# Kernel tuning notes

Hardware: AMD Instinct MI355X
Metric: run time of the kernel (lower is better)

## Reference

```python
import jax, jax.numpy as jnp
import numpy as np

L = 3          # layers
D = 256        # hidden_dim
H = 4          # heads
F = 1024       # ffn_size
IMG = (64, 32) # img_dim
S = IMG[0] * IMG[1]
DK = D // H    # key/query head dim
V = 2 * D      # double_v_dim value dim
DV = V // H    # value head dim
B = 2


def _rel_pos():
    # rotary angles, repeated pairwise as in get_rel_pos
    angle = 1.0 / (10000.0 ** jnp.linspace(0.0, 1.0, DK // 2))
    angle = jnp.repeat(angle, 2)                                  # [DK]
    idx = jnp.arange(S, dtype=jnp.float32)
    sin = jnp.sin(idx[:, None] * angle[None, :])                  # [S, DK]
    cos = jnp.cos(idx[:, None] * angle[None, :])
    # per-head causal decay mask, row-normalized by sqrt(rowsum)
    decay = jnp.log(1.0 - 2.0 ** (-5.0 - jnp.arange(H, dtype=jnp.float32)))  # [H]
    diff = idx[:, None] - idx[None, :]                            # [S, S]
    mask = jnp.where(diff >= 0, jnp.exp(diff[None, :, :] * decay[:, None, None]), 0.0)
    mask = mask / jnp.sqrt(mask.sum(-1, keepdims=True))           # [H, S, S]
    return sin, cos, mask


def _theta_shift(x, sin, cos):
    # x: [B, H, S, DK]; rotate-every-two rotary embedding
    x1, x2 = x[..., ::2], x[..., 1::2]
    rot = jnp.stack([-x2, x1], axis=-1).reshape(x.shape)
    return x * cos + rot * sin


def _ln(x, w, b, eps=1e-5):
    mu = x.mean(-1, keepdims=True)
    var = ((x - mu) ** 2).mean(-1, keepdims=True)
    return (x - mu) / jnp.sqrt(var + eps) * w + b


def _retention(x, sin, cos, mask, Wq, Wk, Wv, Wg, Wo):
    b, s, _ = x.shape
    q = (x @ Wq).reshape(b, s, H, DK).transpose(0, 2, 1, 3)
    k = (x @ Wk).reshape(b, s, H, DK).transpose(0, 2, 1, 3) * (DK ** -0.5)
    v = (x @ Wv).reshape(b, s, H, DV).transpose(0, 2, 1, 3)
    g = x @ Wg                                                    # [b, s, V]
    qr = _theta_shift(q, sin, cos)
    kr = _theta_shift(k, sin, cos)
    qk = jnp.einsum('bhsd,bhtd->bhst', qr, kr) * mask[None]
    denom = jnp.clip(jnp.abs(qk).sum(-1, keepdims=True), 1.0, None)
    qk = qk / jax.lax.stop_gradient(denom)
    o = jnp.einsum('bhst,bhtv->bhsv', qk, v)                      # [b, H, s, DV]
    o = o * jax.lax.rsqrt((o ** 2).mean(-1, keepdims=True) + 1e-6)  # per-head RMSNorm
    o = o.transpose(0, 2, 1, 3).reshape(b, s, V)
    o = (g * jax.nn.sigmoid(g)) * o                               # swish gate
    return o @ Wo


def setup_inputs():
    key = jax.random.key(0)
    ks = jax.random.split(key, 16)
    sc = 0.02
    return {
        'x': jax.random.normal(ks[0], (B, S, D), jnp.float32),
        'Wq': jax.random.normal(ks[1], (L, D, D), jnp.float32) * sc,
        'Wk': jax.random.normal(ks[2], (L, D, D), jnp.float32) * sc,
        'Wv': jax.random.normal(ks[3], (L, D, V), jnp.float32) * sc,
        'Wg': jax.random.normal(ks[4], (L, D, V), jnp.float32) * sc,
        'Wo': jax.random.normal(ks[5], (L, V, D), jnp.float32) * sc,
        'ln1_w': jnp.ones((L, D), jnp.float32),
        'ln1_b': jnp.zeros((L, D), jnp.float32),
        'ln2_w': jnp.ones((L, D), jnp.float32),
        'ln2_b': jnp.zeros((L, D), jnp.float32),
        'W1': jax.random.normal(ks[6], (L, D, F), jnp.float32) * sc,
        'b1': jnp.zeros((L, F), jnp.float32),
        'W2': jax.random.normal(ks[7], (L, F, D), jnp.float32) * sc,
        'b2': jnp.zeros((L, D), jnp.float32),
    }


def reference(x, Wq, Wk, Wv, Wg, Wo, ln1_w, ln1_b, ln2_w, ln2_b, W1, b1, W2, b2):
    sin, cos, mask = _rel_pos()
    for i in range(L):
        y = _retention(_ln(x, ln1_w[i], ln1_b[i]), sin, cos, mask,
                       Wq[i], Wk[i], Wv[i], Wg[i], Wo[i]) + x
        h = _ln(y, ln2_w[i], ln2_b[i])
        x = (jax.nn.gelu(h @ W1[i] + b1[i], approximate=False) @ W2[i] + b2[i]) + y
    return x.reshape(x.shape[0], IMG[0], IMG[1], D)
```

## Files before the change

kernel.cpp:

```cpp
#include <hip/hip_runtime.h>
#include <hip/hip_bf16.h>
#include <cstddef>
#include <cmath>
#include <algorithm>

#define SEQ 2048
#define DMODEL 256
#define NHEAD 4
#define DK 64
#define VDIM 512
#define DV 128
#define NB 2
#define FDIM 1024
#define NROWS (NB*SEQ)
#define QKVGN 1536
#define NSLOT 144

typedef unsigned short u16;
typedef __attribute__((ext_vector_type(8))) short short8;
typedef __attribute__((ext_vector_type(4))) short short4v;
typedef __attribute__((ext_vector_type(4))) float f32x4;

static __device__ __forceinline__ u16 f2b(float f) {
    union { float f; unsigned u; } c; c.f = f;
    unsigned r = c.u + 0x7fffu + ((c.u >> 16) & 1u);
    return (u16)(r >> 16);
}
static __device__ __forceinline__ float b2f(u16 u) {
    union { unsigned u; float f; } c; c.u = ((unsigned)u) << 16; return c.f;
}

static __device__ __forceinline__ f32x4 mfma16_bf16(short4v a, short4v b, f32x4 c) {
    return __builtin_amdgcn_mfma_f32_16x16x16bf16_1k(a, b, c, 0, 0, 0);
}

static __device__ __forceinline__ short4v pack_bf16x4(float a0, float a1, float a2, float a3) {
    union { short4v v; unsigned u[2]; } z;
    union { __hip_bfloat162 h; unsigned u; } p0, p1;
    p0.h = __float22bfloat162_rn(make_float2(a0, a1));
    p1.h = __float22bfloat162_rn(make_float2(a2, a3));
    z.u[0] = p0.u; z.u[1] = p1.u;
    return z.v;
}

#define GLOAD_LDS16(GP, LP) \
    __builtin_amdgcn_global_load_lds((const __attribute__((address_space(1))) void*)(GP), \
                                     (__attribute__((address_space(3))) void*)(LP), 16, 0, 0)

__global__ void tables_kernel(float* __restrict__ sint, float* __restrict__ cost)
{
    int idx = blockIdx.x * 256 + threadIdx.x;
    if (idx >= SEQ * DK) return;
    int s = idx >> 6, d = idx & 63;
    int j = d >> 1;
    float a = powf(10000.f, -(float)j / 31.f);
    float arg = (float)s * a;
    sint[idx] = sinf(arg);
    cost[idx] = cosf(arg);
}

__global__ __launch_bounds__(256) void wconv_kernel(const float* __restrict__ in,
                                                    u16* __restrict__ out, int K, int N,
                                                    size_t in_lstride, size_t out_lstride)
{
    __shared__ float tile[32][33];
    int n0 = blockIdx.x * 32, k0 = blockIdx.y * 32;
    const float* inz = in + (size_t)blockIdx.z * in_lstride;
    u16* outz = out + (size_t)blockIdx.z * out_lstride;
    int tx = threadIdx.x, ty = threadIdx.y;
    #pragma unroll
    for (int r = 0; r < 4; ++r) {
        int kr = ty + r * 8;
        tile[kr][tx] = inz[(size_t)(k0 + kr) * N + n0 + tx];
    }
    __syncthreads();
    #pragma unroll
    for (int r = 0; r < 4; ++r) {
        int nr = ty + r * 8;
        outz[(size_t)(n0 + nr) * K + k0 + tx] = f2b(tile[tx][nr]);
    }
}

__global__ __launch_bounds__(256) void ln_kernel(const float* __restrict__ x,
                                                 const float* __restrict__ w,
                                                 const float* __restrict__ b,
                                                 u16* __restrict__ o)
{
    int row = blockIdx.x;
    int t = threadIdx.x;
    float v = x[(size_t)row * DMODEL + t];
    __shared__ float red[256];
    red[t] = v; __syncthreads();
    for (int st = 128; st > 0; st >>= 1) { if (t < st) red[t] += red[t + st]; __syncthreads(); }
    float mu = red[0] * (1.f / DMODEL);
    __syncthreads();
    red[t] = v * v; __syncthreads();
    for (int st = 128; st > 0; st >>= 1) { if (t < st) red[t] += red[t + st]; __syncthreads(); }
    float var = red[0] * (1.f / DMODEL) - mu * mu;
    o[(size_t)row * DMODEL + t] = f2b((v - mu) * rsqrtf(var + 1e-5f) * w[t] + b[t]);
}

template<int NPART, int HASBIAS>
__global__ __launch_bounds__(256) void lncomb_kernel(const u16* __restrict__ pW,
                                                     const float* __restrict__ bias,
                                                     const float* __restrict__ res,
                                                     const float* __restrict__ w,
                                                     const float* __restrict__ b,
                                                     float* __restrict__ yout,
                                                     u16* __restrict__ o)
{
    int row = blockIdx.x;
    int t = threadIdx.x;
    size_t i = (size_t)row * DMODEL + t;
    const size_t PS = (size_t)NROWS * DMODEL;
    float v = res[i];
    #pragma unroll
    for (int k = 0; k < NPART; ++k) v += b2f(pW[i + k * PS]);
    if (HASBIAS) v += bias[t];
    yout[i] = v;
    __shared__ float red[256];
    red[t] = v; __syncthreads();
    for (int st = 128; st > 0; st >>= 1) { if (t < st) red[t] += red[t + st]; __syncthreads(); }
    float mu = red[0] * (1.f / DMODEL);
    __syncthreads();
    red[t] = v * v; __syncthreads();
    for (int st = 128; st > 0; st >>= 1) { if (t < st) red[t] += red[t + st]; __syncthreads(); }
    float var = red[0] * (1.f / DMODEL) - mu * mu;
    o[i] = f2b((v - mu) * rsqrtf(var + 1e-5f) * w[t] + b[t]);
}

__global__ __launch_bounds__(256) void comb4_kernel(const u16* __restrict__ pW,
                                                    const float* __restrict__ bias,
                                                    const float* __restrict__ yb,
                                                    float* __restrict__ out)
{
    int row = blockIdx.x;
    int t = threadIdx.x;
    size_t i = (size_t)row * DMODEL + t;
    const size_t PS = (size_t)NROWS * DMODEL;
    out[i] = b2f(pW[i]) + b2f(pW[i + PS]) + b2f(pW[i + 2 * PS]) + b2f(pW[i + 3 * PS]) + bias[t] + yb[i];
}

template<int BIAS, int GELU, int ROT, int OUTBF, int SPLIT, int VT>
__global__ __launch_bounds__(256) void gemm64(const u16* __restrict__ A,
                                              const u16* __restrict__ Bt,
                                              void* __restrict__ Cout,
                                              const float* __restrict__ bias,
                                              const float* __restrict__ sint,
                                              const float* __restrict__ cost,
                                              u16* __restrict__ vtout,
                                              int M, int N, int K, int kslice)
{
    __shared__ __align__(16) u16 As[64 * 64];
    __shared__ __align__(16) u16 Bs[64 * 64];
    int bx = blockIdx.x, by = blockIdx.y;
    int tid = threadIdx.x;
    int wave = tid >> 6, lane = tid & 63;
    int wm = wave & 1, wn = wave >> 1;
    int l15 = lane & 15, lg = lane >> 4;
    int kb0 = SPLIT ? blockIdx.z * kslice : 0;
    int kcnt = SPLIT ? kslice : K;

    int L0 = wave * 64 + lane;
    int r0 = L0 >> 3, c0g = (L0 & 7) ^ ((r0 >> 1) & 7);
    int L1 = 256 + wave * 64 + lane;
    int r1 = L1 >> 3, c1g = (L1 & 7) ^ ((r1 >> 1) & 7);
    const u16* Ag0 = A + (size_t)(by * 64 + r0) * K + kb0 + c0g * 8;
    const u16* Ag1 = A + (size_t)(by * 64 + r1) * K + kb0 + c1g * 8;
    const u16* Bg0 = Bt + (size_t)(bx * 64 + r0) * K + kb0 + c0g * 8;
    const u16* Bg1 = Bt + (size_t)(bx * 64 + r1) * K + kb0 + c1g * 8;
    u16* Asw0 = &As[wave * 512];
    u16* Asw1 = &As[2048 + wave * 512];
    u16* Bsw0 = &Bs[wave * 512];
    u16* Bsw1 = &Bs[2048 + wave * 512];

    f32x4 acc[2][2] = {};
    for (int k0 = 0; k0 < kcnt; k0 += 64) {
        GLOAD_LDS16(Ag0 + k0, Asw0);
        GLOAD_LDS16(Ag1 + k0, Asw1);
        GLOAD_LDS16(Bg0 + k0, Bsw0);
        GLOAD_LDS16(Bg1 + k0, Bsw1);
        __syncthreads();
        #pragma unroll
        for (int kk = 0; kk < 2; ++kk) {
            short8 af[2], bf[2];
            #pragma unroll
            for (int i = 0; i < 2; ++i) {
                int ra = wm * 32 + i * 16 + l15;
                int rb = wn * 32 + i * 16 + l15;
                af[i] = *(const short8*)&As[ra * 64 + ((kk * 4 + lg) ^ ((ra >> 1) & 7)) * 8];
                bf[i] = *(const short8*)&Bs[rb * 64 + ((kk * 4 + lg) ^ ((rb >> 1) & 7)) * 8];
            }
            #pragma unroll
            for (int mi = 0; mi < 2; ++mi)
                #pragma unroll
                for (int ni = 0; ni < 2; ++ni)
                    acc[mi][ni] = __builtin_amdgcn_mfma_f32_16x16x32_bf16(af[mi], bf[ni], acc[mi][ni], 0, 0, 0);
        }
        __syncthreads();
    }

    float* Cf = (float*)Cout;
    u16* Ch = (u16*)Cout;
    u16* Chs = (u16*)Cout;
    #pragma unroll
    for (int mi = 0; mi < 2; ++mi)
        #pragma unroll
        for (int ni = 0; ni < 2; ++ni) {
            int colb = bx * 64 + wn * 32 + ni * 16;
            if (VT && colb >= 512 && colb < 1024) {
                int col = colb + l15;
                int z = ((by >> 5) << 2) + ((col - 512) >> 7);
                int dv = (col - 512) & 127;
                int s0b = (by * 64 + wm * 32) & (SEQ - 1);
                short4v pk = pack_bf16x4(acc[mi][ni][0], acc[mi][ni][1], acc[mi][ni][2], acc[mi][ni][3]);
                *(short4v*)(vtout + (size_t)(z * DV + dv) * SEQ + s0b + lg * 8 + mi * 4) = pk;
            } else {
                #pragma unroll
                for (int r = 0; r < 4; ++r) {
                    int row = by * 64 + wm * 32 + mi * 16 + lg * 4 + r;
                    int col = colb + l15;
                    float v = acc[mi][ni][r];
                    if (ROT) {
                        float pv = __shfl_xor(v, 1);
                        if (col < 512) {
                            int s = row & (SEQ - 1);
                            int dk = col & 63;
                            float c = cost[(s << 6) + dk], sn = sint[(s << 6) + dk];
                            float rv = (col & 1) ? (v * c + pv * sn) : (v * c - pv * sn);
                            v = (col < 256) ? rv : rv * 0.125f;
                        }
                    }
                    if (BIAS) v += bias[col];
                    if (GELU) v = 0.5f * v * (1.f + erff(v * 0.70710678118654752f));
                    if (SPLIT)      Chs[(size_t)blockIdx.z * M * N + (size_t)row * N + col] = f2b(v);
                    else if (OUTBF) Ch[(size_t)row * N + col] = f2b(v);
                    else            Cf[(size_t)row * N + col] = v;
                }
            }
        }
}

__global__ __launch_bounds__(256) void retention_p1(
    const u16* __restrict__ qkvg, const u16* __restrict__ vt,
    u16* __restrict__ po, float* __restrict__ pden)
{
    __shared__ __align__(16) u16 Klds[2][2048];
    __shared__ __align__(16) u16 Vlds[2][4096];

    int bid = blockIdx.x;
    int bh = bid & 7;
    int f = bid >> 3;
    int a = 0, base = 0;
    while (f >= base + 4 * (a + 1)) { base += 4 * (a + 1); ++a; }
    int segs = f - base;
    int qt64 = 4 * a + segs / (a + 1);
    int ch = segs % (a + 1);
    int b = bh >> 2, h = bh & 3;
    int slot = bh * NSLOT + f;

    int tid = threadIdx.x;
    int wave = tid >> 6, lane = tid & 63;
    int wq = wave;
    int l15 = lane & 15, lg = lane >> 4;

    float rgeo = 1.f - exp2f(-5.f - (float)h);
    float dec2 = log2f(rgeo);
    float step = exp2f(dec2 * -32.f);

    const u16* qbase  = qkvg + (size_t)b * SEQ * QKVGN + h * 64;
    const u16* kbase  = qbase + 256;
    const u16* vtg    = vt + (size_t)bh * DV * SEQ;

    int q0w = qt64 * 64 + wq * 16;
    short8 qf0 = *(const short8*)(qbase + (size_t)(q0w + l15) * QKVGN + lg * 8);
    short8 qf1 = *(const short8*)(qbase + (size_t)(q0w + l15) * QKVGN + 32 + lg * 8);

    int tb = ch * 8;
    int t_last = (ch == a) ? (2 * qt64 + 1) : (tb + 7);
    int hasdiag = (ch == a);

    float rinv  = exp2f(-dec2);
    float r16   = exp2f(dec2 * -16.f);
    float et00 = exp2f(dec2 * -(float)(tb * 32 + lg * 4));
    float et01 = et00 * rinv;
    float et02 = et01 * rinv;
    float et03 = et02 * rinv;
    float et10 = et00 * r16, et11 = et01 * r16, et12 = et02 * r16, et13 = et03 * r16;

    f32x4 oacc0 = {0.f,0.f,0.f,0.f}, oacc1 = {0.f,0.f,0.f,0.f};
    f32x4 oacc2 = {0.f,0.f,0.f,0.f}, oacc3 = {0.f,0.f,0.f,0.f};
    f32x4 oacc4 = {0.f,0.f,0.f,0.f}, oacc5 = {0.f,0.f,0.f,0.f};
    f32x4 oacc6 = {0.f,0.f,0.f,0.f}, oacc7 = {0.f,0.f,0.f,0.f};
    float den_l = 0.f;

#define STAGE(BUF, TI) do { \
    int t0_ = (TI) * 32; \
    _Pragma("unroll") \
    for (int ii = 0; ii < 3; ++ii) { \
        int inst_ = wave * 3 + ii; \
        if (inst_ < 4) { \
            const u16* g_ = kbase + (size_t)(t0_ + (lane & 31)) * QKVGN + (2 * inst_ + (lane >> 5)) * 8; \
            GLOAD_LDS16(g_, &Klds[BUF][inst_ * 512]); \
        } else { \
            int j_ = inst_ - 4; \
            const u16* g_ = vtg + (size_t)(j_ * 16 + (lane >> 2)) * SEQ + t0_ + (lane & 3) * 8; \
            GLOAD_LDS16(g_, &Vlds[BUF][j_ * 512]); \
        } \
    } \
} while (0)

#define PVSTEP(PA, SEL0, SEL1, SEL2, SEL3, SEL4, SEL5, SEL6, SEL7) do { \
    oacc0 = mfma16_bf16(PA, __builtin_shufflevector(V0, V0, SEL0, SEL1, SEL2, SEL3), oacc0); \
    oacc1 = mfma16_bf16(PA, __builtin_shufflevector(V1, V1, SEL0, SEL1, SEL2, SEL3), oacc1); \
    oacc2 = mfma16_bf16(PA, __builtin_shufflevector(V2, V2, SEL0, SEL1, SEL2, SEL3), oacc2); \
    oacc3 = mfma16_bf16(PA, __builtin_shufflevector(V3, V3, SEL0, SEL1, SEL2, SEL3), oacc3); \
    oacc4 = mfma16_bf16(PA, __builtin_shufflevector(V4, V4, SEL0, SEL1, SEL2, SEL3), oacc4); \
    oacc5 = mfma16_bf16(PA, __builtin_shufflevector(V5, V5, SEL0, SEL1, SEL2, SEL3), oacc5); \
    oacc6 = mfma16_bf16(PA, __builtin_shufflevector(V6, V6, SEL0, SEL1, SEL2, SEL3), oacc6); \
    oacc7 = mfma16_bf16(PA, __builtin_shufflevector(V7, V7, SEL0, SEL1, SEL2, SEL3), oacc7); \
} while (0)

#define BODY(BUF, T0, DIAG) do { \
    const u16* kb_ = &Klds[BUF][0]; \
    const u16* vb_ = &Vlds[BUF][0]; \
    short8 k00 = *(const short8*)(kb_ + (lg    ) * 256 + l15 * 8); \
    short8 k01 = *(const short8*)(kb_ + (4 + lg) * 256 + l15 * 8); \
    short8 k10 = *(const short8*)(kb_ + (lg    ) * 256 + (16 + l15) * 8); \
    short8 k11 = *(const short8*)(kb_ + (4 + lg) * 256 + (16 + l15) * 8); \
    short8 V0 = *(const short8*)(vb_ + (      l15) * 32 + lg * 8); \
    short8 V1 = *(const short8*)(vb_ + (16 +  l15) * 32 + lg * 8); \
    short8 V2 = *(const short8*)(vb_ + (32 +  l15) * 32 + lg * 8); \
    short8 V3 = *(const short8*)(vb_ + (48 +  l15) * 32 + lg * 8); \
    short8 V4 = *(const short8*)(vb_ + (64 +  l15) * 32 + lg * 8); \
    short8 V5 = *(const short8*)(vb_ + (80 +  l15) * 32 + lg * 8); \
    short8 V6 = *(const short8*)(vb_ + (96 +  l15) * 32 + lg * 8); \
    short8 V7 = *(const short8*)(vb_ + (112 + l15) * 32 + lg * 8); \
    f32x4 s0 = {0.f,0.f,0.f,0.f}, s1 = {0.f,0.f,0.f,0.f}; \
    s0 = __builtin_amdgcn_mfma_f32_16x16x32_bf16(k00, qf0, s0, 0, 0, 0); \
    s0 = __builtin_amdgcn_mfma_f32_16x16x32_bf16(k01, qf1, s0, 0, 0, 0); \
    s1 = __builtin_amdgcn_mfma_f32_16x16x32_bf16(k10, qf0, s1, 0, 0, 0); \
    s1 = __builtin_amdgcn_mfma_f32_16x16x32_bf16(k11, qf1, s1, 0, 0, 0); \
    float a0 = s0[0] * et00, a1 = s0[1] * et01, a2 = s0[2] * et02, a3 = s0[3] * et03; \
    float c0 = s1[0] * et10, c1 = s1[1] * et11, c2 = s1[2] * et12, c3 = s1[3] * et13; \
    if (DIAG) { \
        int qr_ = q0w + l15; \
        int tg_ = (T0) + lg * 4; \
        a0 = (tg_ +  0 <= qr_) ? a0 : 0.f;  a1 = (tg_ +  1 <= qr_) ? a1 : 0.f; \
        a2 = (tg_ +  2 <= qr_) ? a2 : 0.f;  a3 = (tg_ +  3 <= qr_) ? a3 : 0.f; \
        c0 = (tg_ + 16 <= qr_) ? c0 : 0.f;  c1 = (tg_ + 17 <= qr_) ? c1 : 0.f; \
        c2 = (tg_ + 18 <= qr_) ? c2 : 0.f;  c3 = (tg_ + 19 <= qr_) ? c3 : 0.f; \
    } \
    den_l += fabsf(a0) + fabsf(a1) + fabsf(a2) + fabsf(a3) \
           + fabsf(c0) + fabsf(c1) + fabsf(c2) + fabsf(c3); \
    short4v pa0 = pack_bf16x4(a0, a1, a2, a3); \
    short4v pa1 = pack_bf16x4(c0, c1, c2, c3); \
    PVSTEP(pa0, 0, 1, 2, 3, 0, 0, 0, 0); \
    PVSTEP(pa1, 4, 5, 6, 7, 0, 0, 0, 0); \
    et00 *= step; et01 *= step; et02 *= step; et03 *= step; \
    et10 *= step; et11 *= step; et12 *= step; et13 *= step; \
} while (0)

    int ti = tb;
    STAGE(0, tb);
    __syncthreads();
    for (; ti + 2 <= t_last; ti += 2) {
        STAGE(1, ti + 1);
        BODY(0, ti * 32, 0);
        __syncthreads();
        STAGE(0, ti + 2);
        BODY(1, (ti + 1) * 32, 0);
        __syncthreads();
    }
    if (ti < t_last) {
        STAGE(1, ti + 1);
        BODY(0, ti * 32, hasdiag);
        __syncthreads();
        BODY(1, (ti + 1) * 32, hasdiag);
    } else {
        BODY(0, ti * 32, hasdiag);
    }
#undef STAGE
#undef PVSTEP
#undef BODY

    den_l += __shfl_xor(den_l, 16);
    den_l += __shfl_xor(den_l, 32);
    if (lane < 16)
        pden[(size_t)slot * 64 + wq * 16 + l15] = den_l;

    u16* pobase = po + (size_t)slot * (64 * 128) + (wq * 16 + lg * 4) * 128 + l15;
    #pragma unroll
    for (int r = 0; r < 4; ++r) {
        pobase[r * 128 +   0] = f2b(oacc0[r]);
        pobase[r * 128 +  16] = f2b(oacc1[r]);
        pobase[r * 128 +  32] = f2b(oacc2[r]);
        pobase[r * 128 +  48] = f2b(oacc3[r]);
        pobase[r * 128 +  64] = f2b(oacc4[r]);
        pobase[r * 128 +  80] = f2b(oacc5[r]);
        pobase[r * 128 +  96] = f2b(oacc6[r]);
        pobase[r * 128 + 112] = f2b(oacc7[r]);
    }
}

__global__ __launch_bounds__(256) void retention_p2(
    const u16* __restrict__ po, const float* __restrict__ pden,
    const u16* __restrict__ qkvg, u16* __restrict__ og)
{
    int bid = blockIdx.x;
    int bh = bid & 7;
    int qt64 = bid >> 3;
    int b = bh >> 2, h = bh & 3;
    int aa = qt64 >> 2, rr = qt64 & 3;
    int sbase = bh * NSLOT + qt64 + 2 * aa * (aa - 1) + rr * aa;
    int nch = aa + 1;
    int t = threadIdx.x;
    int row = t >> 2, c0 = (t & 3) * 32;
    int q = qt64 * 64 + row;

    float den = 0.f;
    for (int k = 0; k < nch; ++k) den += pden[(size_t)(sbase + k) * 64 + row];
    float acc[32];
    #pragma unroll
    for (int j = 0; j < 32; ++j) acc[j] = 0.f;
    for (int k = 0; k < nch; ++k) {
        const u16* p = po + (size_t)(sbase + k) * (64 * 128) + row * 128 + c0;
        #pragma unroll
        for (int j = 0; j < 32; ++j) acc[j] += b2f(p[j]);
    }
    float rgeo = 1.f - exp2f(-5.f - (float)h);
    float dec2 = log2f(rgeo);
    float rp1 = exp2f(dec2 * (float)(q + 1));
    float cs = (1.f - rp1) / (1.f - rgeo);
    float invs = rsqrtf(cs);
    float eqv = exp2f(dec2 * (float)q);
    float d = fmaxf(den * eqv * invs, 1.f);
    float scl = eqv * invs / d;
    float ss = 0.f;
    #pragma unroll
    for (int j = 0; j < 32; ++j) { float v = acc[j] * scl; acc[j] = v; ss += v * v; }
    ss += __shfl_xor(ss, 1); ss += __shfl_xor(ss, 2);
    float rms = rsqrtf(ss * (1.f / DV) + 1e-6f);

    const u16* gbase = qkvg + ((size_t)(b * SEQ + q)) * QKVGN + 1024 + h * DV + c0;
    u16* obase = og + ((size_t)(b * SEQ + q)) * VDIM + h * DV + c0;
    #pragma unroll
    for (int j = 0; j < 32; ++j) {
        float gv = b2f(gbase[j]);
        float sig = 1.f / (1.f + __expf(-gv));
        obase[j] = f2b(gv * sig * acc[j] * rms);
    }
}

extern "C" void kernel_launch(void* const* d_in, const int* in_sizes, int n_in,
                              void* d_out, int out_size, void* d_ws, size_t ws_size,
                              hipStream_t stream)
{
    const float* x0    = (const float*)d_in[0];
    const float* Wq    = (const float*)d_in[1];
    const float* Wk    = (const float*)d_in[2];
    const float* Wv    = (const float*)d_in[3];
    const float* Wg    = (const float*)d_in[4];
    const float* Wo    = (const float*)d_in[5];
    const float* ln1w  = (const float*)d_in[6];
    const float* ln1b  = (const float*)d_in[7];
    const float* ln2w  = (const float*)d_in[8];
    const float* ln2b  = (const float*)d_in[9];
    const float* W1    = (const float*)d_in[10];
    const float* b1    = (const float*)d_in[11];
    const float* W2    = (const float*)d_in[12];
    const float* b2    = (const float*)d_in[13];

    char* ws = (char*)d_ws;
    size_t off = 0;
    auto alloc = [&](size_t bytes) { char* p = ws + off; off += (bytes + 255) & ~(size_t)255; return p; };

    float* sin_t = (float*)alloc(SEQ * DK * 4);
    float* cos_t = (float*)alloc(SEQ * DK * 4);
    u16* wqkvg_t = (u16*)alloc((size_t)3 * QKVGN * DMODEL * 2);
    u16* wo_t    = (u16*)alloc((size_t)3 * DMODEL * VDIM * 2);
    u16* w1_t    = (u16*)alloc((size_t)3 * FDIM * DMODEL * 2);
    u16* w2_t    = (u16*)alloc((size_t)3 * DMODEL * FDIM * 2);
    u16* qkvg    = (u16*)alloc((size_t)NROWS * QKVGN * 2);
    u16* xln     = (u16*)alloc((size_t)NROWS * DMODEL * 2);
    u16* vt      = (u16*)alloc((size_t)NB * NHEAD * DV * SEQ * 2);
    float* yb    = (float*)alloc((size_t)NROWS * DMODEL * 4);
    float* xbuf  = (float*)alloc((size_t)NROWS * DMODEL * 4);
    u16* po      = (u16*)alloc((size_t)8 * NSLOT * 64 * 128 * 2);
    float* pden  = (float*)alloc((size_t)8 * NSLOT * 64 * 4);
    u16* ff1 = qkvg;
    u16* h2  = xln;
    u16* ogb = vt;
    u16* pWh = po;

    tables_kernel<<<(SEQ * DK + 255) / 256, 256, 0, stream>>>(sin_t, cos_t);
    dim3 tb(32, 8);
    const size_t WLQ = (size_t)QKVGN * DMODEL;
    wconv_kernel<<<dim3(8, 8, 3),  tb, 0, stream>>>(Wq, wqkvg_t,              DMODEL, DMODEL, (size_t)DMODEL*DMODEL, WLQ);
    wconv_kernel<<<dim3(8, 8, 3),  tb, 0, stream>>>(Wk, wqkvg_t + 256 * 256,  DMODEL, DMODEL, (size_t)DMODEL*DMODEL, WLQ);
    wconv_kernel<<<dim3(16, 8, 3), tb, 0, stream>>>(Wv, wqkvg_t + 512 * 256,  DMODEL, VDIM,   (size_t)DMODEL*VDIM,   WLQ);
    wconv_kernel<<<dim3(16, 8, 3), tb, 0, stream>>>(Wg, wqkvg_t + 1024 * 256, DMODEL, VDIM,   (size_t)DMODEL*VDIM,   WLQ);
    wconv_kernel<<<dim3(8, 16, 3), tb, 0, stream>>>(Wo, wo_t, VDIM,   DMODEL, (size_t)VDIM*DMODEL,   (size_t)VDIM*DMODEL);
    wconv_kernel<<<dim3(32, 8, 3), tb, 0, stream>>>(W1, w1_t, DMODEL, FDIM,   (size_t)DMODEL*FDIM,   (size_t)DMODEL*FDIM);
    wconv_kernel<<<dim3(8, 32, 3), tb, 0, stream>>>(W2, w2_t, FDIM,   DMODEL, (size_t)FDIM*DMODEL,   (size_t)FDIM*DMODEL);

    ln_kernel<<<NROWS, 256, 0, stream>>>(x0, ln1w, ln1b, xln);

    const float* xres = x0;
    for (int i = 0; i < 3; ++i) {
        const u16* wqkvgi = wqkvg_t + (size_t)i * QKVGN * DMODEL;
        const u16* woi = wo_t + (size_t)i * DMODEL * VDIM;
        const u16* w1i = w1_t + (size_t)i * FDIM * DMODEL;
        const u16* w2i = w2_t + (size_t)i * DMODEL * FDIM;

        gemm64<0,0,1,1,0,1><<<dim3(QKVGN/64, NROWS/64), 256, 0, stream>>>(
            xln, wqkvgi, qkvg, nullptr, sin_t, cos_t, vt, NROWS, QKVGN, DMODEL, 0);

        retention_p1<<<dim3(NSLOT * NB * NHEAD), 256, 0, stream>>>(qkvg, vt, po, pden);
        retention_p2<<<dim3((SEQ/64) * NB * NHEAD), 256, 0, stream>>>(po, pden, qkvg, ogb);

        gemm64<0,0,0,0,1,0><<<dim3(DMODEL/64, NROWS/64, 4), 256, 0, stream>>>(
            ogb, woi, pWh, nullptr, nullptr, nullptr, nullptr, NROWS, DMODEL, VDIM, 128);
        lncomb_kernel<4,0><<<NROWS, 256, 0, stream>>>(pWh, nullptr, xres,
            ln2w + i * DMODEL, ln2b + i * DMODEL, yb, h2);

        gemm64<1,1,0,1,0,0><<<dim3(FDIM/64, NROWS/64), 256, 0, stream>>>(
            h2, w1i, ff1, b1 + (size_t)i * FDIM, nullptr, nullptr, nullptr, NROWS, FDIM, DMODEL, 0);

        gemm64<0,0,0,0,1,0><<<dim3(DMODEL/64, NROWS/64, 4), 256, 0, stream>>>(
            ff1, w2i, pWh, nullptr, nullptr, nullptr, nullptr, NROWS, DMODEL, FDIM, 256);

        if (i < 2) {
            lncomb_kernel<4,1><<<NROWS, 256, 0, stream>>>(pWh, b2 + (size_t)i * DMODEL, yb,
                ln1w + (i + 1) * DMODEL, ln1b + (i + 1) * DMODEL, xbuf, xln);
            xres = xbuf;
        } else {
            comb4_kernel<<<NROWS, 256, 0, stream>>>(pWh, b2 + (size_t)i * DMODEL, yb, (float*)d_out);
        }
    }
}
```

Before: 276.0 us.

## Split retention waves over query pairs and value halves with swizzled V LDS

Each wave now covers 32 query rows and half of the 128 value columns, where before it covered 16 rows and all columns. This halves the V fragments each wave reads from LDS per step, at the cost of computing QK scores twice (once per value-half wave). The V tile is also XOR-swizzled when staged into LDS and when read back, to cut LDS bank conflicts. The MFMA count per wave stays similar, but redundant QK work and register pressure both go up.

```diff
diff --git a/kernel.cpp b/kernel.cpp
--- a/kernel.cpp
+++ b/kernel.cpp
@@ -261,7 +261,7 @@
 
     int tid = threadIdx.x;
     int wave = tid >> 6, lane = tid & 63;
-    int wq = wave;
+    int wq = wave >> 1, wv = wave & 1;
     int l15 = lane & 15, lg = lane >> 4;
 
     float rgeo = 1.f - exp2f(-5.f - (float)h);
@@ -272,9 +272,11 @@
     const u16* kbase  = qbase + 256;
     const u16* vtg    = vt + (size_t)bh * DV * SEQ;
 
-    int q0w = qt64 * 64 + wq * 16;
-    short8 qf0 = *(const short8*)(qbase + (size_t)(q0w + l15) * QKVGN + lg * 8);
-    short8 qf1 = *(const short8*)(qbase + (size_t)(q0w + l15) * QKVGN + 32 + lg * 8);
+    int q0w = qt64 * 64 + wq * 32;
+    short8 qf00 = *(const short8*)(qbase + (size_t)(q0w + l15) * QKVGN + lg * 8);
+    short8 qf01 = *(const short8*)(qbase + (size_t)(q0w + l15) * QKVGN + 32 + lg * 8);
+    short8 qf10 = *(const short8*)(qbase + (size_t)(q0w + 16 + l15) * QKVGN + lg * 8);
+    short8 qf11 = *(const short8*)(qbase + (size_t)(q0w + 16 + l15) * QKVGN + 32 + lg * 8);
 
     int tb = ch * 8;
     int t_last = (ch == a) ? (2 * qt64 + 1) : (tb + 7);
@@ -288,11 +290,11 @@
     float et03 = et02 * rinv;
     float et10 = et00 * r16, et11 = et01 * r16, et12 = et02 * r16, et13 = et03 * r16;
 
-    f32x4 oacc0 = {0.f,0.f,0.f,0.f}, oacc1 = {0.f,0.f,0.f,0.f};
-    f32x4 oacc2 = {0.f,0.f,0.f,0.f}, oacc3 = {0.f,0.f,0.f,0.f};
-    f32x4 oacc4 = {0.f,0.f,0.f,0.f}, oacc5 = {0.f,0.f,0.f,0.f};
-    f32x4 oacc6 = {0.f,0.f,0.f,0.f}, oacc7 = {0.f,0.f,0.f,0.f};
-    float den_l = 0.f;
+    f32x4 o00 = {0.f,0.f,0.f,0.f}, o01 = {0.f,0.f,0.f,0.f};
+    f32x4 o02 = {0.f,0.f,0.f,0.f}, o03 = {0.f,0.f,0.f,0.f};
+    f32x4 o10 = {0.f,0.f,0.f,0.f}, o11 = {0.f,0.f,0.f,0.f};
+    f32x4 o12 = {0.f,0.f,0.f,0.f}, o13 = {0.f,0.f,0.f,0.f};
+    float den0 = 0.f, den1 = 0.f;
 
 #define STAGE(BUF, TI) do { \
     int t0_ = (TI) * 32; \
@@ -304,21 +306,10 @@
             GLOAD_LDS16(g_, &Klds[BUF][inst_ * 512]); \
         } else { \
             int j_ = inst_ - 4; \
-            const u16* g_ = vtg + (size_t)(j_ * 16 + (lane >> 2)) * SEQ + t0_ + (lane & 3) * 8; \
+            const u16* g_ = vtg + (size_t)(j_ * 16 + (lane >> 2)) * SEQ + t0_ + (((lane & 3) ^ ((lane >> 2) & 3)) * 8); \
             GLOAD_LDS16(g_, &Vlds[BUF][j_ * 512]); \
         } \
     } \
-} while (0)
-
-#define PVSTEP(PA, SEL0, SEL1, SEL2, SEL3, SEL4, SEL5, SEL6, SEL7) do { \
-    oacc0 = mfma16_bf16(PA, __builtin_shufflevector(V0, V0, SEL0, SEL1, SEL2, SEL3), oacc0); \
-    oacc1 = mfma16_bf16(PA, __builtin_shufflevector(V1, V1, SEL0, SEL1, SEL2, SEL3), oacc1); \
-    oacc2 = mfma16_bf16(PA, __builtin_shufflevector(V2, V2, SEL0, SEL1, SEL2, SEL3), oacc2); \
-    oacc3 = mfma16_bf16(PA, __builtin_shufflevector(V3, V3, SEL0, SEL1, SEL2, SEL3), oacc3); \
-    oacc4 = mfma16_bf16(PA, __builtin_shufflevector(V4, V4, SEL0, SEL1, SEL2, SEL3), oacc4); \
-    oacc5 = mfma16_bf16(PA, __builtin_shufflevector(V5, V5, SEL0, SEL1, SEL2, SEL3), oacc5); \
-    oacc6 = mfma16_bf16(PA, __builtin_shufflevector(V6, V6, SEL0, SEL1, SEL2, SEL3), oacc6); \
-    oacc7 = mfma16_bf16(PA, __builtin_shufflevector(V7, V7, SEL0, SEL1, SEL2, SEL3), oacc7); \
 } while (0)
 
 #define BODY(BUF, T0, DIAG) do { \
@@ -328,35 +319,53 @@
     short8 k01 = *(const short8*)(kb_ + (4 + lg) * 256 + l15 * 8); \
     short8 k10 = *(const short8*)(kb_ + (lg    ) * 256 + (16 + l15) * 8); \
     short8 k11 = *(const short8*)(kb_ + (4 + lg) * 256 + (16 + l15) * 8); \
-    short8 V0 = *(const short8*)(vb_ + (      l15) * 32 + lg * 8); \
-    short8 V1 = *(const short8*)(vb_ + (16 +  l15) * 32 + lg * 8); \
-    short8 V2 = *(const short8*)(vb_ + (32 +  l15) * 32 + lg * 8); \
-    short8 V3 = *(const short8*)(vb_ + (48 +  l15) * 32 + lg * 8); \
-    short8 V4 = *(const short8*)(vb_ + (64 +  l15) * 32 + lg * 8); \
-    short8 V5 = *(const short8*)(vb_ + (80 +  l15) * 32 + lg * 8); \
-    short8 V6 = *(const short8*)(vb_ + (96 +  l15) * 32 + lg * 8); \
-    short8 V7 = *(const short8*)(vb_ + (112 + l15) * 32 + lg * 8); \
-    f32x4 s0 = {0.f,0.f,0.f,0.f}, s1 = {0.f,0.f,0.f,0.f}; \
-    s0 = __builtin_amdgcn_mfma_f32_16x16x32_bf16(k00, qf0, s0, 0, 0, 0); \
-    s0 = __builtin_amdgcn_mfma_f32_16x16x32_bf16(k01, qf1, s0, 0, 0, 0); \
-    s1 = __builtin_amdgcn_mfma_f32_16x16x32_bf16(k10, qf0, s1, 0, 0, 0); \
-    s1 = __builtin_amdgcn_mfma_f32_16x16x32_bf16(k11, qf1, s1, 0, 0, 0); \
-    float a0 = s0[0] * et00, a1 = s0[1] * et01, a2 = s0[2] * et02, a3 = s0[3] * et03; \
-    float c0 = s1[0] * et10, c1 = s1[1] * et11, c2 = s1[2] * et12, c3 = s1[3] * et13; \
+    int vsw_ = (lg ^ (l15 & 3)) * 8; \
+    short8 V0 = *(const short8*)(vb_ + (wv * 64 +      l15) * 32 + vsw_); \
+    short8 V1 = *(const short8*)(vb_ + (wv * 64 + 16 + l15) * 32 + vsw_); \
+    short8 V2 = *(const short8*)(vb_ + (wv * 64 + 32 + l15) * 32 + vsw_); \
+    short8 V3 = *(const short8*)(vb_ + (wv * 64 + 48 + l15) * 32 + vsw_); \
+    f32x4 s00 = {0.f,0.f,0.f,0.f}, s01 = {0.f,0.f,0.f,0.f}; \
+    f32x4 s10 = {0.f,0.f,0.f,0.f}, s11 = {0.f,0.f,0.f,0.f}; \
+    s00 = __builtin_amdgcn_mfma_f32_16x16x32_bf16(k00, qf00, s00, 0, 0, 0); \
+    s00 = __builtin_amdgcn_mfma_f32_16x16x32_bf16(k01, qf01, s00, 0, 0, 0); \
+    s01 = __builtin_amdgcn_mfma_f32_16x16x32_bf16(k10, qf00, s01, 0, 0, 0); \
+    s01 = __builtin_amdgcn_mfma_f32_16x16x32_bf16(k11, qf01, s01, 0, 0, 0); \
+    s10 = __builtin_amdgcn_mfma_f32_16x16x32_bf16(k00, qf10, s10, 0, 0, 0); \
+    s10 = __builtin_amdgcn_mfma_f32_16x16x32_bf16(k01, qf11, s10, 0, 0, 0); \
+    s11 = __builtin_amdgcn_mfma_f32_16x16x32_bf16(k10, qf10, s11, 0, 0, 0); \
+    s11 = __builtin_amdgcn_mfma_f32_16x16x32_bf16(k11, qf11, s11, 0, 0, 0); \
+    float a0 = s00[0]*et00, a1 = s00[1]*et01, a2 = s00[2]*et02, a3 = s00[3]*et03; \
+    float c0 = s01[0]*et10, c1 = s01[1]*et11, c2 = s01[2]*et12, c3 = s01[3]*et13; \
+    float e0 = s10[0]*et00, e1 = s10[1]*et01, e2 = s10[2]*et02, e3 = s10[3]*et03; \
+    float g0 = s11[0]*et10, g1 = s11[1]*et11, g2 = s11[2]*et12, g3 = s11[3]*et13; \
     if (DIAG) { \
-        int qr_ = q0w + l15; \
+        int qr0_ = q0w + l15, qr1_ = q0w + 16 + l15; \
         int tg_ = (T0) + lg * 4; \
-        a0 = (tg_ +  0 <= qr_) ? a0 : 0.f;  a1 = (tg_ +  1 <= qr_) ? a1 : 0.f; \
-        a2 = (tg_ +  2 <= qr_) ? a2 : 0.f;  a3 = (tg_ +  3 <= qr_) ? a3 : 0.f; \
-        c0 = (tg_ + 16 <= qr_) ? c0 : 0.f;  c1 = (tg_ + 17 <= qr_) ? c1 : 0.f; \
-        c2 = (tg_ + 18 <= qr_) ? c2 : 0.f;  c3 = (tg_ + 19 <= qr_) ? c3 : 0.f; \
+        a0 = (tg_ +  0 <= qr0_) ? a0 : 0.f;  a1 = (tg_ +  1 <= qr0_) ? a1 : 0.f; \
+        a2 = (tg_ +  2 <= qr0_) ? a2 : 0.f;  a3 = (tg_ +  3 <= qr0_) ? a3 : 0.f; \
+        c0 = (tg_ + 16 <= qr0_) ? c0 : 0.f;  c1 = (tg_ + 17 <= qr0_) ? c1 : 0.f; \
+        c2 = (tg_ + 18 <= qr0_) ? c2 : 0.f;  c3 = (tg_ + 19 <= qr0_) ? c3 : 0.f; \
+        e0 = (tg_ +  0 <= qr1_) ? e0 : 0.f;  e1 = (tg_ +  1 <= qr1_) ? e1 : 0.f; \
+        e2 = (tg_ +  2 <= qr1_) ? e2 : 0.f;  e3 = (tg_ +  3 <= qr1_) ? e3 : 0.f; \
+        g0 = (tg_ + 16 <= qr1_) ? g0 : 0.f;  g1 = (tg_ + 17 <= qr1_) ? g1 : 0.f; \
+        g2 = (tg_ + 18 <= qr1_) ? g2 : 0.f;  g3 = (tg_ + 19 <= qr1_) ? g3 : 0.f; \
     } \
-    den_l += fabsf(a0) + fabsf(a1) + fabsf(a2) + fabsf(a3) \
-           + fabsf(c0) + fabsf(c1) + fabsf(c2) + fabsf(c3); \
-    short4v pa0 = pack_bf16x4(a0, a1, a2, a3); \
-    short4v pa1 = pack_bf16x4(c0, c1, c2, c3); \
-    PVSTEP(pa0, 0, 1, 2, 3, 0, 0, 0, 0); \
-    PVSTEP(pa1, 4, 5, 6, 7, 0, 0, 0, 0); \
+    den0 += fabsf(a0)+fabsf(a1)+fabsf(a2)+fabsf(a3)+fabsf(c0)+fabsf(c1)+fabsf(c2)+fabsf(c3); \
+    den1 += fabsf(e0)+fabsf(e1)+fabsf(e2)+fabsf(e3)+fabsf(g0)+fabsf(g1)+fabsf(g2)+fabsf(g3); \
+    short4v pa00 = pack_bf16x4(a0, a1, a2, a3), pa01 = pack_bf16x4(c0, c1, c2, c3); \
+    short4v pa10 = pack_bf16x4(e0, e1, e2, e3), pa11 = pack_bf16x4(g0, g1, g2, g3); \
+    short4v v0l = __builtin_shufflevector(V0, V0, 0, 1, 2, 3), v0h = __builtin_shufflevector(V0, V0, 4, 5, 6, 7); \
+    short4v v1l = __builtin_shufflevector(V1, V1, 0, 1, 2, 3), v1h = __builtin_shufflevector(V1, V1, 4, 5, 6, 7); \
+    short4v v2l = __builtin_shufflevector(V2, V2, 0, 1, 2, 3), v2h = __builtin_shufflevector(V2, V2, 4, 5, 6, 7); \
+    short4v v3l = __builtin_shufflevector(V3, V3, 0, 1, 2, 3), v3h = __builtin_shufflevector(V3, V3, 4, 5, 6, 7); \
+    o00 = mfma16_bf16(pa00, v0l, o00); o00 = mfma16_bf16(pa01, v0h, o00); \
+    o01 = mfma16_bf16(pa00, v1l, o01); o01 = mfma16_bf16(pa01, v1h, o01); \
+    o02 = mfma16_bf16(pa00, v2l, o02); o02 = mfma16_bf16(pa01, v2h, o02); \
+    o03 = mfma16_bf16(pa00, v3l, o03); o03 = mfma16_bf16(pa01, v3h, o03); \
+    o10 = mfma16_bf16(pa10, v0l, o10); o10 = mfma16_bf16(pa11, v0h, o10); \
+    o11 = mfma16_bf16(pa10, v1l, o11); o11 = mfma16_bf16(pa11, v1h, o11); \
+    o12 = mfma16_bf16(pa10, v2l, o12); o12 = mfma16_bf16(pa11, v2h, o12); \
+    o13 = mfma16_bf16(pa10, v3l, o13); o13 = mfma16_bf16(pa11, v3h, o13); \
     et00 *= step; et01 *= step; et02 *= step; et03 *= step; \
     et10 *= step; et11 *= step; et12 *= step; et13 *= step; \
 } while (0)
@@ -381,25 +390,26 @@
         BODY(0, ti * 32, hasdiag);
     }
 #undef STAGE
-#undef PVSTEP
 #undef BODY
 
-    den_l += __shfl_xor(den_l, 16);
-    den_l += __shfl_xor(den_l, 32);
-    if (lane < 16)
-        pden[(size_t)slot * 64 + wq * 16 + l15] = den_l;
-
-    u16* pobase = po + (size_t)slot * (64 * 128) + (wq * 16 + lg * 4) * 128 + l15;
+    den0 += __shfl_xor(den0, 16); den0 += __shfl_xor(den0, 32);
+    den1 += __shfl_xor(den1, 16); den1 += __shfl_xor(den1, 32);
+    if (lane < 16) {
+        pden[(size_t)slot * 64 + wq * 32 + l15] = den0;
+        pden[(size_t)slot * 64 + wq * 32 + 16 + l15] = den1;
+    }
+
+    u16* pobase = po + (size_t)slot * (64 * 128) + (wq * 32 + lg * 4) * 128 + wv * 64 + l15;
     #pragma unroll
     for (int r = 0; r < 4; ++r) {
-        pobase[r * 128 +   0] = f2b(oacc0[r]);
-        pobase[r * 128 +  16] = f2b(oacc1[r]);
-        pobase[r * 128 +  32] = f2b(oacc2[r]);
-        pobase[r * 128 +  48] = f2b(oacc3[r]);
-        pobase[r * 128 +  64] = f2b(oacc4[r]);
-        pobase[r * 128 +  80] = f2b(oacc5[r]);
-        pobase[r * 128 +  96] = f2b(oacc6[r]);
-        pobase[r * 128 + 112] = f2b(oacc7[r]);
+        pobase[r * 128 +  0] = f2b(o00[r]);
+        pobase[r * 128 + 16] = f2b(o01[r]);
+        pobase[r * 128 + 32] = f2b(o02[r]);
+        pobase[r * 128 + 48] = f2b(o03[r]);
+        pobase[16 * 128 + r * 128 +  0] = f2b(o10[r]);
+        pobase[16 * 128 + r * 128 + 16] = f2b(o11[r]);
+        pobase[16 * 128 + r * 128 + 32] = f2b(o12[r]);
+        pobase[16 * 128 + r * 128 + 48] = f2b(o13[r]);
     }
 }
 
```

Measured after the change: 295.9 us. +7.2%, slower.
